# Kernel tuning notes

Measured on AMD Instinct MI355X. Metric: run time of the kernel, lower is better.

The kernel has to match this reference:

```python
import jax, jax.numpy as jnp
import numpy as np

B, T, D = 4, 2048, 1024
H, Dh = 16, 64


def setup_inputs() -> dict:
    key = jax.random.key(0)
    ks = jax.random.split(key, 5)
    # kaiming_normal_ on [H, Dh, D]: fan_in = Dh*D (torch default fan_in over dims[1:]),
    # std = sqrt(2/fan_in); exact init distribution does not affect correctness checks.
    std_qkv = float(np.sqrt(2.0 / (Dh * D)))
    std_o = float(np.sqrt(2.0 / (D * Dh)))
    return {
        "x": jax.random.normal(ks[0], (B, T, D), dtype=jnp.float32),
        "W_Q": jax.random.normal(ks[1], (H, Dh, D), dtype=jnp.float32) * std_qkv,
        "b_Q": jnp.zeros((H, Dh), dtype=jnp.float32),
        "W_K": jax.random.normal(ks[2], (H, Dh, D), dtype=jnp.float32) * std_qkv,
        "b_K": jnp.zeros((H, Dh), dtype=jnp.float32),
        "W_V": jax.random.normal(ks[3], (H, Dh, D), dtype=jnp.float32) * std_qkv,
        "b_V": jnp.zeros((H, Dh), dtype=jnp.float32),
        "W_O": jax.random.normal(ks[4], (H, D, Dh), dtype=jnp.float32) * std_o,
        "b_O": jnp.zeros((D,), dtype=jnp.float32),
    }


def reference(x, W_Q, b_Q, W_K, b_K, W_V, b_V, W_O, b_O):
    # Q/K/V: [batch, tok, heads, d_head]
    Q = jnp.einsum("btd,hkd->bthk", x, W_Q) + b_Q
    K = jnp.einsum("btd,hkd->bthk", x, W_K) + b_K
    V = jnp.einsum("btd,hkd->bthk", x, W_V) + b_V
    d_head = W_Q.shape[1]
    # scores: [batch, heads, tok_Q, tok_K]
    scores = jnp.einsum("bqhk,bshk->bhqs", Q, K) / jnp.sqrt(jnp.asarray(d_head, x.dtype))
    attn = jax.nn.softmax(scores, axis=-1)
    # out per head: [batch, tok_Q, heads, d_head]
    out_h = jnp.einsum("bhqs,bshk->bqhk", attn, V)
    # project back: [batch, tok, d_model]
    return jnp.einsum("bqhk,hdk->bqd", out_h, W_O) + b_O
```

## Files before the change

### kernel.cpp

```cpp
#include <hip/hip_runtime.h>
#include <stdint.h>


typedef __attribute__((ext_vector_type(8))) short bf16x8;
typedef __attribute__((ext_vector_type(4))) float f32x4;

#define MFMA32 __builtin_amdgcn_mfma_f32_16x16x32_bf16

#if __has_builtin(__builtin_amdgcn_exp2f)
#define EXP2(x) __builtin_amdgcn_exp2f(x)
#else
#define EXP2(x) exp2f(x)
#endif

__device__ __forceinline__ unsigned short f2bf(float f) {
  union { float f; unsigned int u; } v; v.f = f;
  unsigned int r = v.u + 0x7FFFu + ((v.u >> 16) & 1u);
  return (unsigned short)(r >> 16);
}

__device__ __forceinline__ void gl_lds16(const void* g, void* l) {
  __builtin_amdgcn_global_load_lds(
      (const __attribute__((address_space(1))) unsigned int*)g,
      (__attribute__((address_space(3))) unsigned int*)l, 16, 0, 0);
}

__device__ __forceinline__ unsigned packbf2(float lo, float hi) {
  union { float f; unsigned u; } a, b; a.f = lo; b.f = hi;
  return __builtin_amdgcn_perm(b.u, a.u, 0x07060302u);
}

__device__ __forceinline__ int rho(int r) { return (r & 3) | ((r >> 1) & 4); }

__device__ __forceinline__ void conv8(const float* __restrict__ src,
                                      unsigned short* __restrict__ dst, int i) {
  const float4* sp = (const float4*)src;
  float4 a = sp[2 * i], b = sp[2 * i + 1];
  union { unsigned short u[8]; uint4 v; } o;
  o.u[0] = f2bf(a.x); o.u[1] = f2bf(a.y); o.u[2] = f2bf(a.z); o.u[3] = f2bf(a.w);
  o.u[4] = f2bf(b.x); o.u[5] = f2bf(b.y); o.u[6] = f2bf(b.z); o.u[7] = f2bf(b.w);
  ((uint4*)dst)[i] = o.v;
}

__global__ __launch_bounds__(256) void prep_all(
    const float* __restrict__ x, const float* __restrict__ WQ,
    const float* __restrict__ WK, const float* __restrict__ WV,
    const float* __restrict__ WO, unsigned short* __restrict__ Xb,
    unsigned short* __restrict__ Wqkv, unsigned short* __restrict__ Wot) {
  const int bx = blockIdx.x, t = threadIdx.x;
  if (bx < 4096) {
    conv8(x, Xb, bx * 256 + t);
  } else if (bx < 4608) {
    conv8(WQ, Wqkv, (bx - 4096) * 256 + t);
  } else if (bx < 5120) {
    conv8(WK, Wqkv + 1048576, (bx - 4608) * 256 + t);
  } else if (bx < 5632) {
    conv8(WV, Wqkv + 2097152, (bx - 5120) * 256 + t);
  } else {
    int tid = (bx - 5632) * 256 + t;
    int h = tid >> 13, rem = tid & 8191;
    int d = rem >> 3, c = rem & 7;
    const float4* sp = (const float4*)(WO + (size_t)h * 65536 + d * 64 + c * 8);
    float4 a = sp[0], e = sp[1];
    union { unsigned short u[8]; uint4 v; } o;
    o.u[0] = f2bf(a.x); o.u[1] = f2bf(a.y); o.u[2] = f2bf(a.z); o.u[3] = f2bf(a.w);
    o.u[4] = f2bf(e.x); o.u[5] = f2bf(e.y); o.u[6] = f2bf(e.z); o.u[7] = f2bf(e.w);
    *(uint4*)(Wot + (size_t)d * 1024 + h * 64 + c * 8) = o.v;
  }
}

__device__ __forceinline__ void gemm_mainloop_1024(
    const unsigned short* __restrict__ A, const unsigned short* __restrict__ B,
    unsigned short* As, unsigned short* Bs, int m0, int n0, f32x4 acc[4][4]) {
  const int tid = threadIdx.x;
  const int lane = tid & 63, w = tid >> 6;
  const int quad = lane >> 4, l15 = lane & 15;
  const int wm = w & 1, wn = w >> 1;
  int srow[4], scl[4];
#pragma unroll
  for (int u = 0; u < 4; ++u) {
    int s = u * 256 + tid;
    srow[u] = s >> 3;
    scl[u] = ((s & 7) ^ ((s >> 3) & 7)) * 8;
  }
  for (int k0 = 0; k0 < 1024; k0 += 64) {
    __syncthreads();
#pragma unroll
    for (int u = 0; u < 4; ++u) {
      int s = u * 256 + tid;
      gl_lds16(A + (size_t)(m0 + srow[u]) * 1024 + k0 + scl[u], As + s * 8);
      gl_lds16(B + (size_t)(n0 + srow[u]) * 1024 + k0 + scl[u], Bs + s * 8);
    }
    __syncthreads();
    bf16x8 af[4][2], bfr[4][2];
#pragma unroll
    for (int i = 0; i < 4; ++i) {
      int ra = wm * 64 + i * 16 + l15;
      int rb = wn * 64 + i * 16 + l15;
#pragma unroll
      for (int c = 0; c < 2; ++c) {
        af[i][c]  = *(const bf16x8*)(As + ra * 64 + (((c * 4 + quad) ^ (ra & 7)) * 8));
        bfr[i][c] = *(const bf16x8*)(Bs + rb * 64 + (((c * 4 + quad) ^ (rb & 7)) * 8));
      }
    }
#pragma unroll
    for (int mi = 0; mi < 4; ++mi)
#pragma unroll
      for (int nj = 0; nj < 4; ++nj) {
        acc[mi][nj] = MFMA32(af[mi][0], bfr[nj][0], acc[mi][nj], 0, 0, 0);
        acc[mi][nj] = MFMA32(af[mi][1], bfr[nj][1], acc[mi][nj], 0, 0, 0);
      }
  }
}

__global__ __launch_bounds__(256) void gemm_qkv(
    const unsigned short* __restrict__ Xb, const unsigned short* __restrict__ Wqkv,
    const float* __restrict__ bQ, const float* __restrict__ bK,
    const float* __restrict__ bV, unsigned short* __restrict__ Qg,
    unsigned short* __restrict__ Kg, unsigned int* __restrict__ Vpg) {
  __shared__ unsigned short As[128 * 64];
  __shared__ unsigned short Bs[128 * 64];
  const int tid = threadIdx.x, lane = tid & 63, w = tid >> 6;
  const int quad = lane >> 4, l15 = lane & 15;
  const int wm = w & 1, wn = w >> 1;
  const int m0 = blockIdx.x * 128, n0 = blockIdx.y * 128;
  f32x4 acc[4][4];
#pragma unroll
  for (int i = 0; i < 4; ++i)
#pragma unroll
    for (int j = 0; j < 4; ++j) acc[i][j] = (f32x4){0.f, 0.f, 0.f, 0.f};

  gemm_mainloop_1024(Xb, Wqkv, As, Bs, m0, n0, acc);

  const int type = n0 >> 10;
  const int nreg = n0 & 1023;
  const float* bias = (type == 0) ? bQ : (type == 1) ? bK : bV;
#pragma unroll
  for (int nj = 0; nj < 4; ++nj) {
    const int n_loc = nreg + wn * 64 + nj * 16 + l15;
    const int h = n_loc >> 6, kh = n_loc & 63;
    const float bv = bias[n_loc];
#pragma unroll
    for (int mi = 0; mi < 4; ++mi) {
      const int mb = m0 + wm * 64 + mi * 16 + quad * 4;
      const int b = mb >> 11, tb = mb & 2047;
      if (type == 2) {
        uint2 pk;
        pk.x = (unsigned)f2bf(acc[mi][nj][0] + bv) |
               ((unsigned)f2bf(acc[mi][nj][1] + bv) << 16);
        pk.y = (unsigned)f2bf(acc[mi][nj][2] + bv) |
               ((unsigned)f2bf(acc[mi][nj][3] + bv) << 16);
        *(uint2*)(Vpg + ((size_t)(b * 16 + h) * 64 + kh) * 1024 + (tb >> 1)) = pk;
      } else {
        unsigned short* dst =
            ((type == 0) ? Qg : Kg) + ((size_t)(b * 16 + h) * 2048 + tb) * 64 + kh;
        const float sc = (type == 0) ? 0.18033688011112042f : 1.0f;
        dst[0]   = f2bf((acc[mi][nj][0] + bv) * sc);
        dst[64]  = f2bf((acc[mi][nj][1] + bv) * sc);
        dst[128] = f2bf((acc[mi][nj][2] + bv) * sc);
        dst[192] = f2bf((acc[mi][nj][3] + bv) * sc);
      }
    }
  }
}

__device__ __forceinline__ void stage_kv(const unsigned short* __restrict__ Kb,
                                         const unsigned int* __restrict__ Vb,
                                         unsigned short* smem, int tid, int s0, int b) {
#pragma unroll
  for (int u = 0; u < 2; ++u) {
    int s = u * 256 + tid, row = s >> 3, g = (s & 7) ^ rho(row);
    gl_lds16(Kb + (size_t)(s0 + row) * 64 + g * 8, smem + b * 8192 + s * 8);
    gl_lds16(Vb + (size_t)row * 1024 + (s0 >> 1) + g * 4,
             smem + b * 8192 + 4096 + s * 8);
  }
}

__global__ __launch_bounds__(256, 2) void flash_attn(
    const unsigned short* __restrict__ Qg, const unsigned short* __restrict__ Kg,
    const unsigned int* __restrict__ Vpg, unsigned short* __restrict__ OH) {
  __shared__ unsigned short smem[16384];
  const int tid = threadIdx.x, lane = tid & 63, w = tid >> 6;
  const int quad = lane >> 4, l15 = lane & 15;
  const int qt = blockIdx.x, bh = blockIdx.y;

  const unsigned short* Qb = Qg + ((size_t)bh * 2048 + qt * 256) * 64;
  const unsigned short* Kb = Kg + (size_t)bh * 2048 * 64;
  const unsigned int*  Vb = Vpg + (size_t)bh * 64 * 1024;

#pragma unroll
  for (int u = 0; u < 8; ++u) {
    int s = u * 256 + tid, row = s >> 3;
    gl_lds16(Qb + row * 64 + ((s & 7) ^ (row & 7)) * 8, smem + s * 8);
  }
  __syncthreads();

  bf16x8 qf[4][2];
#pragma unroll
  for (int qi = 0; qi < 4; ++qi) {
    int row = w * 64 + qi * 16 + l15;
#pragma unroll
    for (int c = 0; c < 2; ++c)
      qf[qi][c] = *(const bf16x8*)(smem + row * 64 + (((c * 4 + quad) ^ (row & 7)) * 8));
  }
  __syncthreads();

  stage_kv(Kb, Vb, smem, tid, 0, 0);

  f32x4 o[4][4];
  float l_part[4] = {0.f, 0.f, 0.f, 0.f};
#pragma unroll
  for (int qi = 0; qi < 4; ++qi)
#pragma unroll
    for (int nj = 0; nj < 4; ++nj) o[qi][nj] = (f32x4){0.f, 0.f, 0.f, 0.f};

  for (int t = 0; t < 32; ++t) {
    __syncthreads();
    if (t < 31) stage_kv(Kb, Vb, smem, tid, (t + 1) * 64, (t + 1) & 1);
    const unsigned short* Kd = smem + (t & 1) * 8192;
    const unsigned short* Vd = Kd + 4096;

#pragma unroll
    for (int blk = 0; blk < 2; ++blk) {
      bf16x8 vb[4];
#pragma unroll
      for (int nj = 0; nj < 4; ++nj) {
        int vrow = nj * 16 + l15;
        vb[nj] = *(const bf16x8*)(Vd + vrow * 64 + (((blk * 4 + quad) ^ rho(vrow)) * 8));
      }
      union { unsigned u[4]; bf16x8 v; } pa[4];
#pragma unroll
      for (int v = 0; v < 2; ++v) {
        int krow = blk * 32 + 8 * (l15 >> 2) + 4 * v + (l15 & 3);
        const unsigned short* kr = Kd + krow * 64;
        bf16x8 ka0 = *(const bf16x8*)(kr + ((quad ^ rho(krow)) * 8));
        bf16x8 ka1 = *(const bf16x8*)(kr + (((4 + quad) ^ rho(krow)) * 8));
#pragma unroll
        for (int qi = 0; qi < 4; ++qi) {
          f32x4 S = (f32x4){0.f, 0.f, 0.f, 0.f};
          S = MFMA32(ka0, qf[qi][0], S, 0, 0, 0);
          S = MFMA32(ka1, qf[qi][1], S, 0, 0, 0);
          float e0 = EXP2(S[0]), e1 = EXP2(S[1]), e2 = EXP2(S[2]), e3 = EXP2(S[3]);
          l_part[qi] += (e0 + e1) + (e2 + e3);
          pa[qi].u[2 * v] = packbf2(e0, e1);
          pa[qi].u[2 * v + 1] = packbf2(e2, e3);
        }
      }
#pragma unroll
      for (int nj = 0; nj < 4; ++nj)
#pragma unroll
        for (int qi = 0; qi < 4; ++qi)
          o[qi][nj] = MFMA32(pa[qi].v, vb[nj], o[qi][nj], 0, 0, 0);
    }
  }

  const int b = bh >> 4, h = bh & 15;
#pragma unroll
  for (int qi = 0; qi < 4; ++qi) {
    float l = l_part[qi];
    l += __shfl_xor(l, 16);
    l += __shfl_xor(l, 32);
    float linv = 1.0f / l;
#pragma unroll
    for (int r = 0; r < 4; ++r) {
      float lr = __shfl(linv, 4 * quad + r);
      int trow = qt * 256 + w * 64 + qi * 16 + 4 * quad + r;
#pragma unroll
      for (int nj = 0; nj < 4; ++nj) {
        int col = h * 64 + nj * 16 + l15;
        OH[((size_t)b * 2048 + trow) * 1024 + col] = f2bf(o[qi][nj][r] * lr);
      }
    }
  }
}

__global__ __launch_bounds__(256) void gemm_o(
    const unsigned short* __restrict__ OHm, const unsigned short* __restrict__ Wot,
    const float* __restrict__ bO, float* __restrict__ Out) {
  __shared__ unsigned short As[128 * 64];
  __shared__ unsigned short Bs[128 * 64];
  const int tid = threadIdx.x, lane = tid & 63, w = tid >> 6;
  const int quad = lane >> 4, l15 = lane & 15;
  const int wm = w & 1, wn = w >> 1;
  const int m0 = blockIdx.x * 128, n0 = blockIdx.y * 128;
  f32x4 acc[4][4];
#pragma unroll
  for (int i = 0; i < 4; ++i)
#pragma unroll
    for (int j = 0; j < 4; ++j) acc[i][j] = (f32x4){0.f, 0.f, 0.f, 0.f};

  gemm_mainloop_1024(OHm, Wot, As, Bs, m0, n0, acc);

#pragma unroll
  for (int nj = 0; nj < 4; ++nj) {
    const int n = n0 + wn * 64 + nj * 16 + l15;
    const float bv = bO[n];
#pragma unroll
    for (int mi = 0; mi < 4; ++mi) {
      const int mb = m0 + wm * 64 + mi * 16 + quad * 4;
#pragma unroll
      for (int r = 0; r < 4; ++r)
        Out[(size_t)(mb + r) * 1024 + n] = acc[mi][nj][r] + bv;
    }
  }
}

extern "C" void kernel_launch(void* const* d_in, const int* in_sizes, int n_in,
                              void* d_out, int out_size, void* d_ws, size_t ws_size,
                              hipStream_t stream) {
  const float* x  = (const float*)d_in[0];
  const float* WQ = (const float*)d_in[1];
  const float* bQ = (const float*)d_in[2];
  const float* WK = (const float*)d_in[3];
  const float* bK = (const float*)d_in[4];
  const float* WV = (const float*)d_in[5];
  const float* bV = (const float*)d_in[6];
  const float* WO = (const float*)d_in[7];
  const float* bO = (const float*)d_in[8];
  float* out = (float*)d_out;

  char* ws = (char*)d_ws;
  unsigned short* Xb   = (unsigned short*)(ws);
  unsigned short* OH   = (unsigned short*)(ws);
  unsigned short* Wqkv = (unsigned short*)(ws + 16777216);
  unsigned short* Wot  = (unsigned short*)(ws + 23068672);
  unsigned short* Qg   = (unsigned short*)(ws + 25165824);
  unsigned short* Kg   = (unsigned short*)(ws + 41943040);
  unsigned int*   Vpg  = (unsigned int*)  (ws + 58720256);

  prep_all<<<6144, 256, 0, stream>>>(x, WQ, WK, WV, WO, Xb, Wqkv, Wot);

  dim3 g1(64, 24);
  gemm_qkv<<<g1, 256, 0, stream>>>(Xb, Wqkv, bQ, bK, bV, Qg, Kg, Vpg);
  dim3 g2(8, 64);
  flash_attn<<<g2, 256, 0, stream>>>(Qg, Kg, Vpg, OH);
  dim3 g3(64, 8);
  gemm_o<<<g3, 256, 0, stream>>>(OH, Wot, bO, out);
}
```

Measured before the change: 273.2 us.

## Shrink output-projection tile to 128x64 and reorder attention grid by head

The output-projection GEMM now uses 128x64 tiles instead of 128x128, with its own single-buffered main loop, which doubles the block count from 512 to 1024 to fill more compute units. The flash-attention grid is transposed so consecutive blocks cover different batch-heads rather than different query tiles of the same head. The smaller GEMM tile lowers per-block register and LDS use but reloads the A tile twice as often and drops whatever pipelining the shared mainloop had. The grid swap changes how K/V reuse in L2 is spread across concurrent blocks.

```diff
diff --git a/kernel.cpp b/kernel.cpp
--- a/kernel.cpp
+++ b/kernel.cpp
@@ -182,7 +182,7 @@
   __shared__ unsigned short smem[16384];
   const int tid = threadIdx.x, lane = tid & 63, w = tid >> 6;
   const int quad = lane >> 4, l15 = lane & 15;
-  const int qt = blockIdx.x, bh = blockIdx.y;
+  const int bh = blockIdx.x, qt = blockIdx.y;
 
   const unsigned short* Qb = Qg + ((size_t)bh * 2048 + qt * 256) * 64;
   const unsigned short* Kb = Kg + (size_t)bh * 2048 * 64;
@@ -278,22 +278,59 @@
     const unsigned short* __restrict__ OHm, const unsigned short* __restrict__ Wot,
     const float* __restrict__ bO, float* __restrict__ Out) {
   __shared__ unsigned short As[128 * 64];
-  __shared__ unsigned short Bs[128 * 64];
+  __shared__ unsigned short Bs[64 * 64];
   const int tid = threadIdx.x, lane = tid & 63, w = tid >> 6;
   const int quad = lane >> 4, l15 = lane & 15;
   const int wm = w & 1, wn = w >> 1;
-  const int m0 = blockIdx.x * 128, n0 = blockIdx.y * 128;
-  f32x4 acc[4][4];
+  const int m0 = blockIdx.x * 128, n0 = blockIdx.y * 64;
+  f32x4 acc[4][2];
 #pragma unroll
   for (int i = 0; i < 4; ++i)
 #pragma unroll
-    for (int j = 0; j < 4; ++j) acc[i][j] = (f32x4){0.f, 0.f, 0.f, 0.f};
-
-  gemm_mainloop_1024(OHm, Wot, As, Bs, m0, n0, acc);
-
-#pragma unroll
-  for (int nj = 0; nj < 4; ++nj) {
-    const int n = n0 + wn * 64 + nj * 16 + l15;
+    for (int j = 0; j < 2; ++j) acc[i][j] = (f32x4){0.f, 0.f, 0.f, 0.f};
+
+  for (int k0 = 0; k0 < 1024; k0 += 64) {
+    __syncthreads();
+#pragma unroll
+    for (int u = 0; u < 4; ++u) {
+      int s = u * 256 + tid, row = s >> 3;
+      int cl = ((s & 7) ^ (row & 7)) * 8;
+      gl_lds16(OHm + (size_t)(m0 + row) * 1024 + k0 + cl, As + s * 8);
+    }
+#pragma unroll
+    for (int u = 0; u < 2; ++u) {
+      int s = u * 256 + tid, row = s >> 3;
+      int cl = ((s & 7) ^ (row & 7)) * 8;
+      gl_lds16(Wot + (size_t)(n0 + row) * 1024 + k0 + cl, Bs + s * 8);
+    }
+    __syncthreads();
+    bf16x8 af[4][2], bfr[2][2];
+#pragma unroll
+    for (int i = 0; i < 4; ++i) {
+      int ra = wm * 64 + i * 16 + l15;
+#pragma unroll
+      for (int c = 0; c < 2; ++c)
+        af[i][c] = *(const bf16x8*)(As + ra * 64 + (((c * 4 + quad) ^ (ra & 7)) * 8));
+    }
+#pragma unroll
+    for (int j = 0; j < 2; ++j) {
+      int rb = wn * 32 + j * 16 + l15;
+#pragma unroll
+      for (int c = 0; c < 2; ++c)
+        bfr[j][c] = *(const bf16x8*)(Bs + rb * 64 + (((c * 4 + quad) ^ (rb & 7)) * 8));
+    }
+#pragma unroll
+    for (int mi = 0; mi < 4; ++mi)
+#pragma unroll
+      for (int nj = 0; nj < 2; ++nj) {
+        acc[mi][nj] = MFMA32(af[mi][0], bfr[nj][0], acc[mi][nj], 0, 0, 0);
+        acc[mi][nj] = MFMA32(af[mi][1], bfr[nj][1], acc[mi][nj], 0, 0, 0);
+      }
+  }
+
+#pragma unroll
+  for (int nj = 0; nj < 2; ++nj) {
+    const int n = n0 + wn * 32 + nj * 16 + l15;
     const float bv = bO[n];
 #pragma unroll
     for (int mi = 0; mi < 4; ++mi) {
@@ -332,8 +369,8 @@
 
   dim3 g1(64, 24);
   gemm_qkv<<<g1, 256, 0, stream>>>(Xb, Wqkv, bQ, bK, bV, Qg, Kg, Vpg);
-  dim3 g2(8, 64);
+  dim3 g2(64, 8);
   flash_attn<<<g2, 256, 0, stream>>>(Qg, Kg, Vpg, OH);
-  dim3 g3(64, 8);
+  dim3 g3(64, 16);
   gemm_o<<<g3, 256, 0, stream>>>(OH, Wot, bO, out);
 }
```

Result: faster. 258.4 us (-5.4%).
